# Kernel optimization log

Measured on AMD Instinct MI355X. Metric: run time of the kernel, lower is better.

Reference implementation:

```python
import jax, jax.numpy as jnp
import numpy as np

B, T = 4, 2048
N_EMBD = 1024
TIME_EMBD = 128
N_HEAD = 16
C_IN = N_EMBD + TIME_EMBD  # 1152


def setup_inputs() -> dict:
    key = jax.random.key(0)
    ks = jax.random.split(key, 7)
    s_in = 1.0 / np.sqrt(C_IN)
    s_e = 1.0 / np.sqrt(N_EMBD)
    return {
        "x": jax.random.normal(ks[0], (B, T, C_IN), jnp.float32),
        "ln_w": jnp.ones((C_IN,), jnp.float32),
        "ln_b": jnp.zeros((C_IN,), jnp.float32),
        "W_attn": jax.random.normal(ks[1], (C_IN, 3 * N_EMBD), jnp.float32) * s_in,
        "b_attn": jax.random.normal(ks[2], (3 * N_EMBD,), jnp.float32) * 0.01,
        "W_proj": jax.random.normal(ks[3], (N_EMBD, N_EMBD), jnp.float32) * s_e,
        "b_proj": jax.random.normal(ks[4], (N_EMBD,), jnp.float32) * 0.01,
    }


def _layernorm(x, w, b, eps=1e-5):
    mu = jnp.mean(x, axis=-1, keepdims=True)
    var = jnp.var(x, axis=-1, keepdims=True)
    return (x - mu) * jax.lax.rsqrt(var + eps) * w + b


def reference(x, ln_w, ln_b, W_attn, b_attn, W_proj, b_proj):
    h = _layernorm(x, ln_w, ln_b)                      # [B,T,C_IN]
    qkv = h @ W_attn + b_attn                          # [B,T,3*N_EMBD]
    q, k, v = jnp.split(qkv, 3, axis=-1)
    hd = N_EMBD // N_HEAD
    q = q.reshape(B, T, N_HEAD, hd).transpose(0, 2, 1, 3)  # [B,H,T,hd]
    k = k.reshape(B, T, N_HEAD, hd).transpose(0, 2, 1, 3)
    v = v.reshape(B, T, N_HEAD, hd).transpose(0, 2, 1, 3)
    att = jnp.einsum("bhqd,bhkd->bhqk", q, k) * (1.0 / np.sqrt(hd))
    mask = jnp.tril(jnp.ones((T, T), bool))
    att = jnp.where(mask, att, -jnp.inf)
    att = jax.nn.softmax(att, axis=-1)                 # dropout p=0 -> identity
    y = jnp.einsum("bhqk,bhkd->bhqd", att, v)          # [B,H,T,hd]
    y = y.transpose(0, 2, 1, 3).reshape(B, T, N_EMBD)
    return y @ W_proj + b_proj
```

## Files before the change

kernel.cpp:

```cpp
#include <hip/hip_runtime.h>
#include <hip/hip_bf16.h>

#define BB 4
#define TT 2048
#define C_IN 1152
#define NE 1024
#define NH 16
#define HD 64
#define MM (BB*TT)
#define N_QKV (3*NE)

typedef __attribute__((ext_vector_type(8))) short s16x8;
typedef __attribute__((ext_vector_type(4))) short s16x4;
typedef __attribute__((ext_vector_type(4))) float f32x4;

static __device__ __forceinline__ unsigned short f2bf(float x) {
    unsigned int u = __float_as_uint(x);
    unsigned int r = (u + 0x7fffu + ((u >> 16) & 1u)) >> 16;
    return (unsigned short)r;
}

static __device__ __forceinline__ void async16(const void* g, void* l) {
    __builtin_amdgcn_global_load_lds((const __attribute__((address_space(1))) void*)g,
                                     (__attribute__((address_space(3))) void*)l, 16, 0, 0);
}

#define TCA_BLOCKS ((N_QKV / 32) * (C_IN / 32))
#define TCP_BLOCKS ((NE / 32) * (NE / 32))
__global__ __launch_bounds__(256) void prep_kernel(const float* __restrict__ x,
                                                   const float* __restrict__ lw,
                                                   const float* __restrict__ lb,
                                                   unsigned short* __restrict__ h,
                                                   const float* __restrict__ Wa,
                                                   unsigned short* __restrict__ Wat,
                                                   const float* __restrict__ Wp,
                                                   unsigned short* __restrict__ Wpt) {
    __shared__ float tile[32][33];
    __shared__ float red[2][4];
    const int bid = blockIdx.x;
    const int tid = threadIdx.x;

    if (bid < MM) {
        const float4* xr = (const float4*)(x + (size_t)bid * C_IN);
        const float4 a0 = xr[tid];
        float4 a1 = make_float4(0.f, 0.f, 0.f, 0.f);
        if (tid < 32) a1 = xr[256 + tid];
        float s  = a0.x + a0.y + a0.z + a0.w + a1.x + a1.y + a1.z + a1.w;
        float sq = a0.x*a0.x + a0.y*a0.y + a0.z*a0.z + a0.w*a0.w
                 + a1.x*a1.x + a1.y*a1.y + a1.z*a1.z + a1.w*a1.w;
        for (int off = 1; off < 64; off <<= 1) {
            s  += __shfl_xor(s, off, 64);
            sq += __shfl_xor(sq, off, 64);
        }
        const int wid = tid >> 6, lane = tid & 63;
        if (lane == 0) { red[0][wid] = s; red[1][wid] = sq; }
        __syncthreads();
        s  = red[0][0] + red[0][1] + red[0][2] + red[0][3];
        sq = red[1][0] + red[1][1] + red[1][2] + red[1][3];
        const float mu  = s * (1.f / C_IN);
        const float var = sq * (1.f / C_IN) - mu * mu;
        const float rs  = rsqrtf(var + 1e-5f);
        const float4* w4 = (const float4*)lw;
        const float4* b4 = (const float4*)lb;
        unsigned short* hr = h + (size_t)bid * C_IN;
        {
            const float4 wv = w4[tid], bv = b4[tid];
            s16x4 o;
            o[0] = (short)f2bf((a0.x - mu) * rs * wv.x + bv.x);
            o[1] = (short)f2bf((a0.y - mu) * rs * wv.y + bv.y);
            o[2] = (short)f2bf((a0.z - mu) * rs * wv.z + bv.z);
            o[3] = (short)f2bf((a0.w - mu) * rs * wv.w + bv.w);
            *(s16x4*)(hr + tid * 4) = o;
        }
        if (tid < 32) {
            const float4 wv = w4[256 + tid], bv = b4[256 + tid];
            s16x4 o;
            o[0] = (short)f2bf((a1.x - mu) * rs * wv.x + bv.x);
            o[1] = (short)f2bf((a1.y - mu) * rs * wv.y + bv.y);
            o[2] = (short)f2bf((a1.z - mu) * rs * wv.z + bv.z);
            o[3] = (short)f2bf((a1.w - mu) * rs * wv.w + bv.w);
            *(s16x4*)(hr + (256 + tid) * 4) = o;
        }
        return;
    }

    const float* in; unsigned short* out; int K, N, n0, k0;
    if (bid < MM + TCA_BLOCKS) {
        const int idx = bid - MM;
        in = Wa; out = Wat; K = C_IN; N = N_QKV;
        n0 = (idx % (N_QKV / 32)) * 32; k0 = (idx / (N_QKV / 32)) * 32;
    } else {
        const int idx = bid - MM - TCA_BLOCKS;
        in = Wp; out = Wpt; K = NE; N = NE;
        n0 = (idx % (NE / 32)) * 32; k0 = (idx / (NE / 32)) * 32;
    }
    const int tx = tid & 31, ty = tid >> 5;
    for (int i = ty; i < 32; i += 8)
        tile[i][tx] = in[(size_t)(k0 + i) * N + n0 + tx];
    __syncthreads();
    for (int i = ty; i < 32; i += 8)
        out[(size_t)(n0 + i) * K + k0 + tx] = f2bf(tile[tx][i]);
}

#define ATT_SC 0.18033688011112042f

#define EP_STRIDE 136
template <int MODE>
__global__ __launch_bounds__(256) void gemm_bt(const unsigned short* __restrict__ A,
                                               const unsigned short* __restrict__ Bt,
                                               const float* __restrict__ bias,
                                               void* __restrict__ outp,
                                               unsigned short* __restrict__ kb,
                                               unsigned short* __restrict__ vt,
                                               int M, int N, int K) {
    constexpr int BN   = (MODE == 0) ? 128 : 64;
    constexpr int NB   = BN / 32;
    constexpr int ABUF = 8192;
    constexpr int BBUF = BN * 64;
    constexpr int BUFS = ABUF + BBUF;
    __shared__ unsigned short smem[2 * BUFS];
    const int tid = threadIdx.x;
    const int wid = tid >> 6, lane = tid & 63;
    const int wm = wid >> 1, wn = wid & 1;
    const int quad = lane >> 4, l16 = lane & 15;

    int m0, n0;
    if (MODE == 0) {
        const int bid = blockIdx.y * gridDim.x + blockIdx.x;
        const int xcd = bid & 7;
        const int k   = bid >> 3;
        const int mg  = k / 96;
        const int r1  = k % 96;
        const int ng  = r1 / 32;
        const int rr  = r1 % 32;
        m0 = (xcd * 8 + mg * 4 + (rr & 3)) * 128;
        n0 = (ng * 8 + (rr >> 2)) * 128;
    } else {
        const int gx  = gridDim.x;
        const int nwg = gx * gridDim.y;
        const int bid = blockIdx.y * gx + blockIdx.x;
        const int wg  = (bid & 7) * (nwg >> 3) + (bid >> 3);
        m0 = (wg / gx) * 128; n0 = (wg % gx) * BN;
    }

    const int rl = lane >> 3;
    const int sc = (lane & 7) ^ rl;
    const int bwid = (MODE == 0) ? wid : (wid & 1);
    const unsigned short* gA = A  + (size_t)(m0 + wid * 32 + rl) * K + sc * 8;
    const unsigned short* gB = Bt + (size_t)(n0 + bwid * 32 + rl) * K + sc * 8;

    f32x4 acc[4][NB] = {};
    const int nk = K >> 6;

    const int sc0 = (quad ^ (l16 & 7)) * 8;
    const int sc1 = ((4 + quad) ^ (l16 & 7)) * 8;

#define STAGE(KT, BUF)                                                          \
    {                                                                           \
        const unsigned short* a_ = gA + (KT) * 64;                              \
        unsigned short* sa_ = &smem[(BUF) * BUFS + wid * 2048];                 \
        _Pragma("unroll")                                                       \
        for (int j = 0; j < 4; j++)                                             \
            async16(a_ + (size_t)(j * 8) * K, sa_ + j * 512);                   \
        if (MODE == 0 || wid < 2) {                                             \
            const unsigned short* b_ = gB + (KT) * 64;                          \
            unsigned short* sb_ = &smem[(BUF) * BUFS + ABUF + wid * 2048];      \
            _Pragma("unroll")                                                   \
            for (int j = 0; j < 4; j++)                                         \
                async16(b_ + (size_t)(j * 8) * K, sb_ + j * 512);               \
        }                                                                       \
    }

    STAGE(0, 0);

    for (int kt = 0; kt < nk; kt++) {
        __syncthreads();
        const int cur = kt & 1;
        if (kt + 1 < nk) STAGE(kt + 1, cur ^ 1);

        const unsigned short* As_ = &smem[cur * BUFS];
        const unsigned short* Bs_ = &smem[cur * BUFS + ABUF];
        #pragma unroll
        for (int h = 0; h < 2; h++) {
            const int sch = h ? sc1 : sc0;
            s16x8 af[4], bfb[NB];
            #pragma unroll
            for (int mi = 0; mi < 4; mi++)
                af[mi] = *(const s16x8*)&As_[(wm * 64 + mi * 16 + l16) * 64 + sch];
            #pragma unroll
            for (int ni = 0; ni < NB; ni++)
                bfb[ni] = *(const s16x8*)&Bs_[(wn * (BN / 2) + ni * 16 + l16) * 64 + sch];
            #pragma unroll
            for (int mi = 0; mi < 4; mi++)
                #pragma unroll
                for (int ni = 0; ni < NB; ni++)
                    acc[mi][ni] = __builtin_amdgcn_mfma_f32_16x16x32_bf16(af[mi], bfb[ni], acc[mi][ni], 0, 0, 0);
        }
    }
#undef STAGE

    const int which0 = n0 >> 10;
    const float sc_ = (MODE == 0 && which0 == 0) ? ATT_SC : 1.0f;
    for (int ni = 0; ni < NB; ni++) {
        const float bv = bias[n0 + wn * (BN / 2) + ni * 16 + l16];
        for (int mi = 0; mi < 4; mi++)
            for (int r = 0; r < 4; r++)
                acc[mi][ni][r] = (acc[mi][ni][r] + bv) * sc_;
    }

    if (MODE == 1) {
        float* Tf = (float*)smem;
        float* out = (float*)outp;
        for (int p = 0; p < 2; p++) {
            __syncthreads();
            if (wm == p) {
                for (int mi = 0; mi < 4; mi++)
                    for (int ni = 0; ni < NB; ni++) {
                        const int col = wn * (BN / 2) + ni * 16 + l16;
                        for (int r = 0; r < 4; r++)
                            Tf[(mi * 16 + quad * 4 + r) * BN + col] = acc[mi][ni][r];
                    }
            }
            __syncthreads();
            const int rlo = tid >> 4;
            const int c4 = (tid & 15) * 4;
            for (int rr2 = rlo; rr2 < 64; rr2 += 16) {
                *(float4*)&out[(size_t)(m0 + p * 64 + rr2) * N + n0 + c4] =
                    *(const float4*)&Tf[rr2 * BN + c4];
            }
        }
        return;
    }

    const int which = n0 >> 10;
    const int bb = m0 >> 11;
    const int mloc = m0 & 2047;
    unsigned short* T = smem;

    __syncthreads();
    if (which < 2) {
        for (int mi = 0; mi < 4; mi++)
            for (int ni = 0; ni < 4; ni++) {
                const int nl = wn * 64 + ni * 16 + l16;
                for (int r = 0; r < 4; r++)
                    T[(wm * 64 + mi * 16 + quad * 4 + r) * EP_STRIDE + nl] = f2bf(acc[mi][ni][r]);
            }
    } else {
        for (int mi = 0; mi < 4; mi++)
            for (int ni = 0; ni < 4; ni++) {
                const int nlh = wn * 64 + ni * 16 + l16;
                const int mlb = wm * 64 + mi * 16 + quad * 4;
                for (int r = 0; r < 4; r += 2) {
                    const unsigned int pk = (unsigned int)f2bf(acc[mi][ni][r]) |
                                            ((unsigned int)f2bf(acc[mi][ni][r + 1]) << 16);
                    *(unsigned int*)&T[nlh * EP_STRIDE + mlb + r] = pk;
                }
            }
    }
    __syncthreads();

    if (which < 2) {
        unsigned short* qk = (which == 0) ? (unsigned short*)outp : kb;
        const int ml = tid >> 2, c = tid & 3;
        const int nl0 = c * 32;
        const int hh = ((n0 & 1023) >> 6) + (nl0 >> 6);
        const int d0 = nl0 & 63;
        for (int half = 0; half < 2; half++) {
            const int row = half * 64 + ml;
            const int t = mloc + row;
            unsigned short* dst = qk + ((size_t)(bb * 16 + hh) * TT + t) * HD + d0;
            const unsigned short* src = &T[row * EP_STRIDE + nl0];
            for (int u = 0; u < 4; u++)
                *(s16x8*)(dst + u * 8) = *(const s16x8*)(src + u * 8);
        }
    } else {
        const int nlh = tid >> 2, c = tid & 3;
        const int hb = (n0 - 2048) >> 6;
        for (int half = 0; half < 2; half++) {
            const int row = half * 64 + nlh;
            unsigned short* dst = vt + ((size_t)(bb * 16 + hb + half) * HD + nlh) * TT + mloc + c * 32;
            const unsigned short* src = &T[row * EP_STRIDE + c * 32];
            for (int u = 0; u < 4; u++)
                *(s16x8*)(dst + u * 8) = *(const s16x8*)(src + u * 8);
        }
    }
}

#define PST 72

__global__ __launch_bounds__(256) void attn_kernel(const unsigned short* __restrict__ qb,
                                                   const unsigned short* __restrict__ kb,
                                                   const unsigned short* __restrict__ vt,
                                                   unsigned short* __restrict__ yb) {
    __shared__ unsigned short Ks[2][64 * 64];
    __shared__ unsigned short Vs[2][64 * 64];
    __shared__ unsigned short Ps[4][2 * 16 * PST];
    const int tid = threadIdx.x, wid = tid >> 6, lane = tid & 63;
    const int quad = lane >> 4, l16 = lane & 15;
    const int bh = blockIdx.x & 63;
    const int qblk = 15 - (blockIdx.x >> 6);

    const unsigned short* qh = qb + (size_t)bh * TT * HD;
    const unsigned short* kh = kb + (size_t)bh * TT * HD;
    const unsigned short* vh = vt + (size_t)bh * HD * TT;
    unsigned short* ps = Ps[wid];

    const int q0w = qblk * 128 + wid * 32;
    s16x8 aq[2][2];
    #pragma unroll
    for (int mf = 0; mf < 2; mf++) {
        aq[mf][0] = *(const s16x8*)&qh[(size_t)(q0w + mf * 16 + l16) * HD + quad * 8];
        aq[mf][1] = *(const s16x8*)&qh[(size_t)(q0w + mf * 16 + l16) * HD + 32 + quad * 8];
    }
    s16x8 onesf;
    #pragma unroll
    for (int i = 0; i < 8; i++) onesf[i] = (short)0x3F80;

    f32x4 yacc[2][4] = {};
    f32x4 lacc[2] = {};
    const int ntiles = 2 * qblk + 2;

    const int rl = lane >> 3;
    const int cc = (lane & 7) ^ (rl & 7);
    const unsigned short* kp0 = kh + (size_t)(wid * 16 + rl) * HD + cc * 8;
    const unsigned short* kp1 = kh + (size_t)(wid * 16 + 8 + rl) * HD + cc * 8;
    const unsigned short* vp0 = vh + (size_t)(wid * 16 + rl) * TT + cc * 8;
    const unsigned short* vp1 = vh + (size_t)(wid * 16 + 8 + rl) * TT + cc * 8;
    const int ldsK0 = wid * 16 * 64, ldsK1 = (wid * 16 + 8) * 64;

    async16(kp0, &Ks[0][ldsK0]);  async16(kp1, &Ks[0][ldsK1]);
    async16(vp0, &Vs[0][ldsK0]);  async16(vp1, &Vs[0][ldsK1]);
    kp0 += 64 * HD; kp1 += 64 * HD; vp0 += 64; vp1 += 64;

    const int p0s = quad ^ (l16 & 7);
    const int p1s = (4 + quad) ^ (l16 & 7);

#define ATT_STEP(CUR, TT_)                                                              \
    {                                                                                   \
        __syncthreads();                                                                \
        if ((TT_) + 1 < ntiles) {                                                       \
            async16(kp0, &Ks[(CUR) ^ 1][ldsK0]);  async16(kp1, &Ks[(CUR) ^ 1][ldsK1]);  \
            async16(vp0, &Vs[(CUR) ^ 1][ldsK0]);  async16(vp1, &Vs[(CUR) ^ 1][ldsK1]);  \
            kp0 += 64 * HD; kp1 += 64 * HD; vp0 += 64; vp1 += 64;                       \
        }                                                                               \
        const int tk0 = (TT_) * 64;                                                     \
        if (tk0 <= q0w + 31) {                                                          \
            const unsigned short* Kc = Ks[CUR];                                         \
            const unsigned short* Vc = Vs[CUR];                                         \
            s16x8 kf[4][2], vf[4][2];                                                   \
            _Pragma("unroll")                                                           \
            for (int nj = 0; nj < 4; nj++) {                                            \
                kf[nj][0] = *(const s16x8*)&Kc[(nj * 16 + l16) * 64 + p0s * 8];         \
                kf[nj][1] = *(const s16x8*)&Kc[(nj * 16 + l16) * 64 + p1s * 8];         \
            }                                                                           \
            _Pragma("unroll")                                                           \
            for (int ni = 0; ni < 4; ni++) {                                            \
                vf[ni][0] = *(const s16x8*)&Vc[(ni * 16 + l16) * 64 + p0s * 8];         \
                vf[ni][1] = *(const s16x8*)&Vc[(ni * 16 + l16) * 64 + p1s * 8];         \
            }                                                                           \
            _Pragma("unroll")                                                           \
            for (int mf = 0; mf < 2; mf++) {                                            \
                const int f0 = q0w + mf * 16;                                           \
                if (tk0 > f0 + 15) continue;                                            \
                unsigned short* pm = ps + mf * (16 * PST);                              \
                const int qg = f0 + l16;                                                \
                f32x4 st[4];                                                            \
                _Pragma("unroll")                                                       \
                for (int nj = 0; nj < 4; nj++) {                                        \
                    f32x4 z = {};                                                       \
                    z = __builtin_amdgcn_mfma_f32_16x16x32_bf16(kf[nj][0], aq[mf][0], z, 0, 0, 0); \
                    z = __builtin_amdgcn_mfma_f32_16x16x32_bf16(kf[nj][1], aq[mf][1], z, 0, 0, 0); \
                    st[nj] = z;                                                         \
                }                                                                       \
                const bool diag = (tk0 + 64 > f0);                                      \
                float pv[4][4];                                                         \
                _Pragma("unroll")                                                       \
                for (int nj = 0; nj < 4; nj++)                                          \
                    _Pragma("unroll")                                                   \
                    for (int r = 0; r < 4; r++)                                         \
                        pv[nj][r] = exp2f(st[nj][r]);                                   \
                if (diag) {                                                             \
                    _Pragma("unroll")                                                   \
                    for (int nj = 0; nj < 4; nj++) {                                    \
                        const int keyb = tk0 + nj * 16 + quad * 4;                      \
                        _Pragma("unroll")                                               \
                        for (int r = 0; r < 4; r++)                                     \
                            if (keyb + r > qg) pv[nj][r] = 0.f;                         \
                    }                                                                   \
                }                                                                       \
                _Pragma("unroll")                                                       \
                for (int nj = 0; nj < 4; nj++) {                                        \
                    const unsigned int pk0 = __builtin_amdgcn_perm(                     \
                        __float_as_uint(pv[nj][1]), __float_as_uint(pv[nj][0]), 0x07060302u); \
                    const unsigned int pk1 = __builtin_amdgcn_perm(                     \
                        __float_as_uint(pv[nj][3]), __float_as_uint(pv[nj][2]), 0x07060302u); \
                    *(uint2*)&pm[l16 * PST + nj * 16 + quad * 4] = make_uint2(pk0, pk1);\
                }                                                                       \
                __asm volatile("s_waitcnt lgkmcnt(0)" ::: "memory");                    \
                __builtin_amdgcn_s_setprio(1);                                          \
                const s16x8 ap0 = *(const s16x8*)&pm[l16 * PST + quad * 8];             \
                const s16x8 ap1 = *(const s16x8*)&pm[l16 * PST + 32 + quad * 8];        \
                lacc[mf] = __builtin_amdgcn_mfma_f32_16x16x32_bf16(ap0, onesf, lacc[mf], 0, 0, 0); \
                lacc[mf] = __builtin_amdgcn_mfma_f32_16x16x32_bf16(ap1, onesf, lacc[mf], 0, 0, 0); \
                _Pragma("unroll")                                                       \
                for (int ni = 0; ni < 4; ni++) {                                        \
                    yacc[mf][ni] = __builtin_amdgcn_mfma_f32_16x16x32_bf16(ap0, vf[ni][0], yacc[mf][ni], 0, 0, 0); \
                    yacc[mf][ni] = __builtin_amdgcn_mfma_f32_16x16x32_bf16(ap1, vf[ni][1], yacc[mf][ni], 0, 0, 0); \
                }                                                                       \
                __builtin_amdgcn_s_setprio(0);                                          \
            }                                                                           \
        }                                                                               \
    }

    for (int t = 0; t < ntiles; t += 2) {
        ATT_STEP(0, t);
        ATT_STEP(1, t + 1);
    }
#undef ATT_STEP

    const int bbi = bh >> 4, hh = bh & 15;
    #pragma unroll
    for (int mf = 0; mf < 2; mf++) {
        float linv[4];
        #pragma unroll
        for (int r = 0; r < 4; r++)
            linv[r] = 1.0f / lacc[mf][r];
        #pragma unroll
        for (int ni = 0; ni < 4; ni++)
            #pragma unroll
            for (int r = 0; r < 4; r++) {
                const int trow = q0w + mf * 16 + quad * 4 + r;
                yb[((size_t)bbi * TT + trow) * NE + hh * HD + ni * 16 + l16] =
                    f2bf(yacc[mf][ni][r] * linv[r]);
            }
    }
}

extern "C" void kernel_launch(void* const* d_in, const int* in_sizes, int n_in,
                              void* d_out, int out_size, void* d_ws, size_t ws_size,
                              hipStream_t stream) {
    const float* x      = (const float*)d_in[0];
    const float* ln_w   = (const float*)d_in[1];
    const float* ln_b   = (const float*)d_in[2];
    const float* W_attn = (const float*)d_in[3];
    const float* b_attn = (const float*)d_in[4];
    const float* W_proj = (const float*)d_in[5];
    const float* b_proj = (const float*)d_in[6];
    float* out = (float*)d_out;

    char* ws = (char*)d_ws;
    unsigned short* h    = (unsigned short*)ws;  ws += (size_t)MM * C_IN * 2;
    unsigned short* Wat  = (unsigned short*)ws;  ws += (size_t)N_QKV * C_IN * 2;
    unsigned short* Wpt  = (unsigned short*)ws;  ws += (size_t)NE * NE * 2;
    unsigned short* qbuf = (unsigned short*)ws;  ws += (size_t)MM * NE * 2;
    unsigned short* kbuf = (unsigned short*)ws;  ws += (size_t)MM * NE * 2;
    unsigned short* vtbf = (unsigned short*)ws;  ws += (size_t)MM * NE * 2;
    unsigned short* ybuf = (unsigned short*)ws;  ws += (size_t)MM * NE * 2;

    prep_kernel<<<MM + TCA_BLOCKS + TCP_BLOCKS, 256, 0, stream>>>(x, ln_w, ln_b, h,
                                                                  W_attn, Wat, W_proj, Wpt);
    gemm_bt<0><<<dim3(N_QKV / 128, MM / 128), 256, 0, stream>>>(h, Wat, b_attn, qbuf, kbuf, vtbf,
                                                                MM, N_QKV, C_IN);
    attn_kernel<<<64 * 16, 256, 0, stream>>>(qbuf, kbuf, vtbf, ybuf);
    gemm_bt<1><<<dim3(NE / 64, MM / 128), 256, 0, stream>>>(ybuf, Wpt, b_proj, out, nullptr, nullptr,
                                                            MM, NE, NE);
}
```

Measured before the change: 284.1 us.

## Split KV range of longest causal query blocks across two blocks and merge

The attention kernel moves to a job table in which query blocks 11–15 have their key range split into two halves, each handled by a separate workgroup. Each half writes fp32 partial outputs and row sums to workspace instead of bf16 results. A new merge kernel adds the two partials and normalises them into the bf16 output. The aim is to even out work across workgroups and shorten the causal tail, at the cost of an extra launch and extra fp32 traffic. The partial buffers reuse the start of the workspace, overlapping the h and Wat buffers, which are no longer needed at that point.

```diff
diff --git a/kernel.cpp b/kernel.cpp
--- a/kernel.cpp
+++ b/kernel.cpp
@@ -287,18 +287,30 @@
 }
 
 #define PST 72
+#define NSPLIT 5
+#define NJOBS 21
+
+__device__ const signed char JQ[NJOBS] = {10,9,8,15,15,14,7,14,13,13,12,6,12,11,11,5,4,3,2,1,0};
+__device__ const signed char JM[NJOBS] = { 0,0,0, 1, 2, 1,0, 2, 1, 2, 1,0, 2, 1, 2,0,0,0,0,0,0};
 
 __global__ __launch_bounds__(256) void attn_kernel(const unsigned short* __restrict__ qb,
                                                    const unsigned short* __restrict__ kb,
                                                    const unsigned short* __restrict__ vt,
-                                                   unsigned short* __restrict__ yb) {
+                                                   unsigned short* __restrict__ yb,
+                                                   float* __restrict__ ypart,
+                                                   float* __restrict__ lpart) {
     __shared__ unsigned short Ks[2][64 * 64];
     __shared__ unsigned short Vs[2][64 * 64];
     __shared__ unsigned short Ps[4][2 * 16 * PST];
     const int tid = threadIdx.x, wid = tid >> 6, lane = tid & 63;
     const int quad = lane >> 4, l16 = lane & 15;
     const int bh = blockIdx.x & 63;
-    const int qblk = 15 - (blockIdx.x >> 6);
+    const int j  = blockIdx.x >> 6;
+    const int qblk = JQ[j];
+    const int mode = JM[j];
+    const int hs = (qblk + 2) & ~1;
+    const int t0 = (mode == 2) ? hs : 0;
+    const int t1 = (mode == 1) ? hs : (2 * qblk + 2);
 
     const unsigned short* qh = qb + (size_t)bh * TT * HD;
     const unsigned short* kh = kb + (size_t)bh * TT * HD;
@@ -318,14 +330,13 @@
 
     f32x4 yacc[2][4] = {};
     f32x4 lacc[2] = {};
-    const int ntiles = 2 * qblk + 2;
 
     const int rl = lane >> 3;
     const int cc = (lane & 7) ^ (rl & 7);
-    const unsigned short* kp0 = kh + (size_t)(wid * 16 + rl) * HD + cc * 8;
-    const unsigned short* kp1 = kh + (size_t)(wid * 16 + 8 + rl) * HD + cc * 8;
-    const unsigned short* vp0 = vh + (size_t)(wid * 16 + rl) * TT + cc * 8;
-    const unsigned short* vp1 = vh + (size_t)(wid * 16 + 8 + rl) * TT + cc * 8;
+    const unsigned short* kp0 = kh + (size_t)(t0 * 64 + wid * 16 + rl) * HD + cc * 8;
+    const unsigned short* kp1 = kh + (size_t)(t0 * 64 + wid * 16 + 8 + rl) * HD + cc * 8;
+    const unsigned short* vp0 = vh + (size_t)(wid * 16 + rl) * TT + t0 * 64 + cc * 8;
+    const unsigned short* vp1 = vh + (size_t)(wid * 16 + 8 + rl) * TT + t0 * 64 + cc * 8;
     const int ldsK0 = wid * 16 * 64, ldsK1 = (wid * 16 + 8) * 64;
 
     async16(kp0, &Ks[0][ldsK0]);  async16(kp1, &Ks[0][ldsK1]);
@@ -338,7 +349,7 @@
 #define ATT_STEP(CUR, TT_)                                                              \
     {                                                                                   \
         __syncthreads();                                                                \
-        if ((TT_) + 1 < ntiles) {                                                       \
+        if ((TT_) + 1 < t1) {                                                           \
             async16(kp0, &Ks[(CUR) ^ 1][ldsK0]);  async16(kp1, &Ks[(CUR) ^ 1][ldsK1]);  \
             async16(vp0, &Vs[(CUR) ^ 1][ldsK0]);  async16(vp1, &Vs[(CUR) ^ 1][ldsK1]);  \
             kp0 += 64 * HD; kp1 += 64 * HD; vp0 += 64; vp1 += 64;                       \
@@ -412,11 +423,34 @@
         }                                                                               \
     }
 
-    for (int t = 0; t < ntiles; t += 2) {
+    for (int t = t0; t < t1; t += 2) {
         ATT_STEP(0, t);
         ATT_STEP(1, t + 1);
     }
 #undef ATT_STEP
+
+    if (mode != 0) {
+        const int qi = qblk - 11;
+        float* yp = ypart + (((size_t)(qi * 2 + (mode - 1)) * 64 + bh) * 128) * 64;
+        #pragma unroll
+        for (int mf = 0; mf < 2; mf++)
+            #pragma unroll
+            for (int ni = 0; ni < 4; ni++)
+                #pragma unroll
+                for (int r = 0; r < 4; r++) {
+                    const int ql = wid * 32 + mf * 16 + quad * 4 + r;
+                    yp[(size_t)ql * 64 + ni * 16 + l16] = yacc[mf][ni][r];
+                }
+        if (l16 == 0) {
+            float* lp = lpart + ((size_t)(qi * 2 + (mode - 1)) * 64 + bh) * 128;
+            #pragma unroll
+            for (int mf = 0; mf < 2; mf++)
+                #pragma unroll
+                for (int r = 0; r < 4; r++)
+                    lp[wid * 32 + mf * 16 + quad * 4 + r] = lacc[mf][r];
+        }
+        return;
+    }
 
     const int bbi = bh >> 4, hh = bh & 15;
     #pragma unroll
@@ -436,6 +470,36 @@
     }
 }
 
+__global__ __launch_bounds__(256) void attn_merge(const float* __restrict__ yp,
+                                                  const float* __restrict__ lp,
+                                                  unsigned short* __restrict__ yb) {
+    const int qi = blockIdx.x >> 6;
+    const int bh = blockIdx.x & 63;
+    const int qblk = 11 + qi;
+    const int bbi = bh >> 4, hh = bh & 15;
+    const float* y0 = yp + (((size_t)(qi * 2 + 0) * 64 + bh) * 128) * 64;
+    const float* y1 = yp + (((size_t)(qi * 2 + 1) * 64 + bh) * 128) * 64;
+    const float* l0 = lp + ((size_t)(qi * 2 + 0) * 64 + bh) * 128;
+    const float* l1 = lp + ((size_t)(qi * 2 + 1) * 64 + bh) * 128;
+    const int tid = threadIdx.x;
+    #pragma unroll
+    for (int i = 0; i < 8; i++) {
+        const int f = tid + i * 256;
+        const int ql = f >> 4;
+        const int d4 = (f & 15) * 4;
+        const float4 a = *(const float4*)&y0[(size_t)ql * 64 + d4];
+        const float4 b = *(const float4*)&y1[(size_t)ql * 64 + d4];
+        const float linv = 1.0f / (l0[ql] + l1[ql]);
+        s16x4 o;
+        o[0] = (short)f2bf((a.x + b.x) * linv);
+        o[1] = (short)f2bf((a.y + b.y) * linv);
+        o[2] = (short)f2bf((a.z + b.z) * linv);
+        o[3] = (short)f2bf((a.w + b.w) * linv);
+        const int trow = qblk * 128 + ql;
+        *(s16x4*)&yb[((size_t)bbi * TT + trow) * NE + hh * HD + d4] = o;
+    }
+}
+
 extern "C" void kernel_launch(void* const* d_in, const int* in_sizes, int n_in,
                               void* d_out, int out_size, void* d_ws, size_t ws_size,
                               hipStream_t stream) {
@@ -457,11 +521,15 @@
     unsigned short* vtbf = (unsigned short*)ws;  ws += (size_t)MM * NE * 2;
     unsigned short* ybuf = (unsigned short*)ws;  ws += (size_t)MM * NE * 2;
 
+    float* ypart = (float*)d_ws;
+    float* lpart = ypart + (size_t)NSPLIT * 2 * 64 * 128 * 64;
+
     prep_kernel<<<MM + TCA_BLOCKS + TCP_BLOCKS, 256, 0, stream>>>(x, ln_w, ln_b, h,
                                                                   W_attn, Wat, W_proj, Wpt);
     gemm_bt<0><<<dim3(N_QKV / 128, MM / 128), 256, 0, stream>>>(h, Wat, b_attn, qbuf, kbuf, vtbf,
                                                                 MM, N_QKV, C_IN);
-    attn_kernel<<<64 * 16, 256, 0, stream>>>(qbuf, kbuf, vtbf, ybuf);
+    attn_kernel<<<NJOBS * 64, 256, 0, stream>>>(qbuf, kbuf, vtbf, ybuf, ypart, lpart);
+    attn_merge<<<NSPLIT * 64, 256, 0, stream>>>(ypart, lpart, ybuf);
     gemm_bt<1><<<dim3(NE / 64, MM / 128), 256, 0, stream>>>(ybuf, Wpt, b_proj, out, nullptr, nullptr,
                                                             MM, NE, NE);
 }
```

Result: no change. 289.8 us (+2.0%).
